# Kernel tuning notes

Measured on AMD Instinct MI355X. Metric: run time of the kernel, lower is better.

The kernel has to match this reference:

```python
import jax, jax.numpy as jnp
import numpy as np
from jax.scipy.special import logsumexp

SINKHORN_ITERS = 10


def _fix_coupling_sinkhorn(lc, lp1, lp2, iterations=SINKHORN_ITERS):
    # lc: [Z,S], lp1: [Z], lp2: [S]
    for _ in range(iterations):
        lc = lc + lp1[:, None] - logsumexp(lc, axis=1, keepdims=True)
        lc = lc + lp2[None, :] - logsumexp(lc, axis=0, keepdims=True)
    return lc


def _fix_coupling_rejection(lc, lp1, lp2):
    fixed_p1 = lc + lp1[:, None] - logsumexp(lc, axis=1, keepdims=True)
    approx_lp2 = logsumexp(fixed_p1, axis=0)
    accept = lp2 - approx_lp2
    accept = accept - jnp.max(accept)
    acc_s2_given_s1 = jax.nn.log_softmax(fixed_p1, axis=-1) + accept[None, :]
    log_keep = logsumexp(acc_s2_given_s1, axis=-1)
    certainly_keep = jnp.exp(log_keep) >= 1.0
    resample = jnp.where(
        certainly_keep, -jnp.inf,
        jnp.log1p(-jnp.where(certainly_keep, 0.0, jnp.exp(log_keep))))
    compensation = resample[:, None] + lp2[None, :]
    return lp1[:, None] + jnp.logaddexp(acc_s2_given_s1, compensation)


def setup_inputs() -> dict:
    key = jax.random.key(0)
    ks = jax.random.split(key, 8)
    B, S, Z, H1, H2 = 64, 512, 1024, 512, 256
    return {
        "s_logits": jax.random.normal(ks[0], (B, S), jnp.float32),
        "W1": jax.random.normal(ks[1], (S, H1), jnp.float32) / np.sqrt(S),
        "b1": jnp.zeros((H1,), jnp.float32),
        "W2": jax.random.normal(ks[2], (H1, H2), jnp.float32) / np.sqrt(H1),
        "b2": jnp.zeros((H2,), jnp.float32),
        "Wout": jax.random.normal(ks[3], (H2, Z, S), jnp.float32) / np.sqrt(H2),
        "bout": jnp.zeros((Z, S), jnp.float32),
        "prior": jax.random.normal(ks[4], (Z,), jnp.float32) * 0.05,
    }


def reference(s_logits, W1, b1, W2, b2, Wout, bout, prior):
    z_logits = jax.nn.log_softmax(prior)  # [Z]

    def get_joint(sl):  # sl: [S]
        v = jax.nn.softmax(sl)
        v = jax.nn.sigmoid(v @ W1 + b1)
        v = jax.nn.sigmoid(v @ W2 + b2)
        log_joint = jnp.einsum('h,hzs->zs', v, Wout) + bout  # [Z,S]
        log_joint = _fix_coupling_sinkhorn(log_joint, z_logits, sl)
        return _fix_coupling_rejection(log_joint, z_logits, sl)

    return jax.vmap(get_joint)(s_logits)  # [B,Z,S]
```

## Files before the change

kernel.cpp:

```cpp
#include <hip/hip_runtime.h>
#include <math.h>

#define Bn 64
#define Sn 512
#define Zn 1024
#define H1n 512
#define H2n 256
#define ZSn (Zn*Sn)

#define OFF_LP1  0
#define OFF_VT   1024
#define OFF_V    17408
#define OFF_W    50176
#define OFF_R    82944
#define OFF_PM   148480
#define OFF_PS   672768
#define OFF_KB   1310720
#define NEED_BF16_BYTES ((size_t)OFF_KB*4 + (size_t)Bn*ZSn*2)

#define NINF (-__builtin_inff())

__device__ __forceinline__ float wred_max(float x){
#pragma unroll
  for (int o=32;o;o>>=1) x = fmaxf(x, __shfl_xor(x, o, 64));
  return x;
}
__device__ __forceinline__ float wred_sum(float x){
#pragma unroll
  for (int o=32;o;o>>=1) x += __shfl_xor(x, o, 64);
  return x;
}
__device__ __forceinline__ float lae(float a, float c){
  float m = fmaxf(a,c), n = fminf(a,c);
  return m + log1pf(__expf(n-m));
}
__device__ __forceinline__ float toF(float v){ return v; }
__device__ __forceinline__ float toF(unsigned short v){ return __uint_as_float(((unsigned int)v)<<16); }
__device__ __forceinline__ unsigned int pack2(float a, float b){
  unsigned int ua = __float_as_uint(a), ub = __float_as_uint(b);
  ua = (ua + 0x7fffu + ((ua>>16)&1u)) >> 16;
  ub = (ub + 0x7fffu + ((ub>>16)&1u)) & 0xffff0000u;
  return ua | ub;
}

__global__ __launch_bounds__(512) void prep_kernel(const float* __restrict__ prior,
                                                   float* __restrict__ ws){
  __shared__ float red[8];
  int t = threadIdx.x;
  float x0 = prior[t], x1 = prior[t+512];
  float m = wred_max(fmaxf(x0,x1));
  if ((t&63)==0) red[t>>6] = m;
  __syncthreads();
  float M = red[0];
#pragma unroll
  for (int i=1;i<8;i++) M = fmaxf(M, red[i]);
  float e = __expf(x0-M)+__expf(x1-M);
  e = wred_sum(e);
  __syncthreads();
  if ((t&63)==0) red[t>>6] = e;
  __syncthreads();
  float T = 0.f;
#pragma unroll
  for (int i=0;i<8;i++) T += red[i];
  float lse = M + logf(T);
  ws[OFF_LP1 + t]       = x0 - lse;
  ws[OFF_LP1 + t + 512] = x1 - lse;
}

__global__ __launch_bounds__(512) void mlp_kernel(const float* __restrict__ sl,
    const float* __restrict__ W1, const float* __restrict__ b1,
    const float* __restrict__ W2, const float* __restrict__ b2,
    float* __restrict__ ws){
  __shared__ float p[Sn];
  __shared__ float h1s[H1n];
  __shared__ float red[8];
  int b = blockIdx.x, t = threadIdx.x;
  float x = sl[b*Sn + t];
  float m = wred_max(x);
  if ((t&63)==0) red[t>>6] = m;
  __syncthreads();
  float M = red[0];
#pragma unroll
  for (int i=1;i<8;i++) M = fmaxf(M, red[i]);
  float e = __expf(x-M);
  float es = wred_sum(e);
  __syncthreads();
  if ((t&63)==0) red[t>>6] = es;
  __syncthreads();
  float T = 0.f;
#pragma unroll
  for (int i=0;i<8;i++) T += red[i];
  p[t] = e / T;
  __syncthreads();
  float acc = b1[t];
#pragma unroll 8
  for (int s=0;s<Sn;s++) acc = fmaf(p[s], W1[s*H1n + t], acc);
  h1s[t] = 1.f/(1.f+__expf(-acc));
  __syncthreads();
  if (t < H2n){
    float a2 = b2[t];
#pragma unroll 8
    for (int s=0;s<H1n;s++) a2 = fmaf(h1s[s], W2[s*H2n + t], a2);
    ws[OFF_VT + t*Bn + b] = 1.f/(1.f+__expf(-a2));
  }
}

template<int BF>
__global__ __launch_bounds__(256,1) void gemm_kernel(const float* __restrict__ Wout,
    const float* __restrict__ bout, const float* __restrict__ ws,
    float* __restrict__ Kf, unsigned int* __restrict__ Kb){
  int zh = blockIdx.x*256 + threadIdx.x;
  const float* __restrict__ VT = ws + OFF_VT;
  float2 acc[Bn];
#pragma unroll
  for (int b=0;b<Bn;b++){ acc[b].x = 0.f; acc[b].y = 0.f; }
  const float2* Wp = (const float2*)Wout;
#pragma unroll 2
  for (int h=0; h<H2n; h++){
    float2 wv = Wp[(size_t)h*(ZSn/2) + zh];
    const float* vh = VT + (h<<6);
#pragma unroll
    for (int b=0;b<Bn;b++){
      acc[b].x = fmaf(vh[b], wv.x, acc[b].x);
      acc[b].y = fmaf(vh[b], wv.y, acc[b].y);
    }
  }
  float2 bb = ((const float2*)bout)[zh];
#pragma unroll
  for (int b=0;b<Bn;b++){
    float ax = acc[b].x + bb.x, ay = acc[b].y + bb.y;
    if (BF){
      Kb[(size_t)b*(ZSn/2) + zh] = pack2(ax, ay);
    } else {
      float2 o; o.x = ax; o.y = ay;
      ((float2*)Kf)[(size_t)b*(ZSn/2) + zh] = o;
    }
  }
}

template<typename KT>
__global__ __launch_bounds__(512) void iter_fused(const KT* __restrict__ Kg,
    float* __restrict__ ws, const float* __restrict__ sl, int iter, int mode){
  __shared__ KT Ksh[64*512];
  __shared__ float vsh[512];
  __shared__ float ush[64];
  __shared__ float lsh[64];
  int t = threadIdx.x;
  int b = blockIdx.x >> 4, c = blockIdx.x & 15;
  const float4* s4 = (const float4*)(Kg + ((size_t)((b<<10) + (c<<6)) << 9));
  float4* d4 = (float4*)Ksh;
  constexpr int NV = (int)sizeof(KT)*4;
#pragma unroll
  for (int i=0;i<NV;i++) d4[i*512 + t] = s4[i*512 + t];
  if (t < 64) lsh[t] = ws[OFF_LP1 + (c<<6) + t];
  float v_s;
  if (iter == 0) v_s = 0.f;
  else {
    float M = NINF, S = 0.f;
#pragma unroll
    for (int cc=0; cc<16; cc++){
      float m = ws[OFF_PM + ((b*16+cc)<<9) + t];
      float p = ws[OFF_PS + ((b*16+cc)<<9) + t];
      float nm = fmaxf(M, m);
      S = S*__expf(M-nm) + p*__expf(m-nm);
      M = nm;
    }
    v_s = sl[(b<<9) + t] - (M + logf(S));
  }
  vsh[t] = v_s;
  if (mode) ws[OFF_V + (b<<9) + t] = v_s;
  __syncthreads();
  int l = t & 63, w = t >> 6;
#pragma unroll
  for (int rr=0; rr<8; rr++){
    int row = (w<<3) + rr;
    float x[8];
    float m = NINF;
#pragma unroll
    for (int j=0;j<8;j++){
      x[j] = toF(Ksh[(row<<9) + (j<<6) + l]) + vsh[(j<<6)+l];
      m = fmaxf(m, x[j]);
    }
    m = wred_max(m);
    float s = 0.f;
#pragma unroll
    for (int j=0;j<8;j++) s += __expf(x[j]-m);
    s = wred_sum(s);
    float L = m + logf(s);
    if (l == 0){
      ush[row] = lsh[row] - L;
      if (mode) ws[OFF_R + (b<<10) + (c<<6) + row] = L;
    }
  }
  __syncthreads();
  float M = NINF, S = 0.f;
#pragma unroll 8
  for (int i=0;i<64;i++){
    float x2 = toF(Ksh[(i<<9) + t]) + ush[i];
    float nm = fmaxf(M, x2);
    S = S*__expf(M-nm) + __expf(x2-nm);
    M = nm;
  }
  ws[OFF_PM + ((b*16+c)<<9) + t] = M;
  ws[OFF_PS + ((b*16+c)<<9) + t] = S;
}

__global__ __launch_bounds__(512) void wker(float* __restrict__ ws, const float* __restrict__ sl){
  __shared__ float red[8];
  int b = blockIdx.x, s = threadIdx.x;
  float M = NINF, S = 0.f;
#pragma unroll
  for (int cc=0; cc<16; cc++){
    float m = ws[OFF_PM + ((b*16+cc)<<9) + s];
    float p = ws[OFF_PS + ((b*16+cc)<<9) + s];
    float nm = fmaxf(M, m);
    S = S*__expf(M-nm) + p*__expf(m-nm);
    M = nm;
  }
  float L = M + logf(S);
  float v = ws[OFF_V + (b<<9) + s];
  float araw = sl[(b<<9)+s] - v - L;
  float mm = wred_max(araw);
  if ((s&63)==0) red[s>>6] = mm;
  __syncthreads();
  float amax = red[0];
#pragma unroll
  for (int i=1;i<8;i++) amax = fmaxf(amax, red[i]);
  ws[OFF_W + (b<<9) + s] = v + araw - amax;
}

template<typename KT>
__global__ __launch_bounds__(512) void final_fused(const KT* Kg,
    float* out, const float* __restrict__ ws, const float* __restrict__ sl){
  int t = threadIdx.x, l = t & 63, wv = t >> 6;
  int row = blockIdx.x*8 + wv;
  int b = row >> 10, z = row & (Zn-1);
  const KT* Kr = Kg + ((size_t)row << 9);
  const float* wr = ws + OFF_W + (b << 9);
  const float* pr = sl + (b << 9);
  float r  = ws[OFF_R + row];
  float l1 = ws[OFF_LP1 + z];
  float k[8], a[8];
  float m = NINF;
#pragma unroll
  for (int j=0;j<8;j++){
    k[j] = toF(Kr[(j<<6)+l]);
    a[j] = k[j] - r + wr[(j<<6)+l];
    m = fmaxf(m, a[j]);
  }
  m = wred_max(m);
  float s = 0.f;
#pragma unroll
  for (int j=0;j<8;j++) s += __expf(a[j]-m);
  s = wred_sum(s);
  float lk = m + logf(s);
  float rs = (lk >= 0.f) ? NINF : log1pf(-__expf(lk));
  float* Or = out + ((size_t)row << 9);
#pragma unroll
  for (int j=0;j<8;j++){
    Or[(j<<6)+l] = l1 + lae(a[j], rs + pr[(j<<6)+l]);
  }
}

extern "C" void kernel_launch(void* const* d_in, const int* in_sizes, int n_in,
                              void* d_out, int out_size, void* d_ws, size_t ws_size,
                              hipStream_t stream) {
  const float* sl    = (const float*)d_in[0];
  const float* W1    = (const float*)d_in[1];
  const float* b1    = (const float*)d_in[2];
  const float* W2    = (const float*)d_in[3];
  const float* b2    = (const float*)d_in[4];
  const float* Wout  = (const float*)d_in[5];
  const float* bout  = (const float*)d_in[6];
  const float* prior = (const float*)d_in[7];
  float* ws = (float*)d_ws;
  float* Kf = (float*)d_out;
  unsigned short* Kb = (unsigned short*)(ws + OFF_KB);
  const bool use_bf16 = (ws_size >= NEED_BF16_BYTES);

  prep_kernel<<<1, 512, 0, stream>>>(prior, ws);
  mlp_kernel<<<Bn, 512, 0, stream>>>(sl, W1, b1, W2, b2, ws);

  if (use_bf16){
    gemm_kernel<1><<<ZSn/512, 256, 0, stream>>>(Wout, bout, ws, nullptr, (unsigned int*)Kb);
    for (int it = 0; it < 10; ++it)
      iter_fused<unsigned short><<<Bn*16, 512, 0, stream>>>(Kb, ws, sl, it, 0);
    iter_fused<unsigned short><<<Bn*16, 512, 0, stream>>>(Kb, ws, sl, 10, 1);
    wker<<<Bn, 512, 0, stream>>>(ws, sl);
    final_fused<unsigned short><<<Bn*Zn/8, 512, 0, stream>>>(Kb, (float*)d_out, ws, sl);
  } else {
    gemm_kernel<0><<<ZSn/512, 256, 0, stream>>>(Wout, bout, ws, Kf, nullptr);
    for (int it = 0; it < 10; ++it)
      iter_fused<float><<<Bn*16, 512, 0, stream>>>(Kf, ws, sl, it, 0);
    iter_fused<float><<<Bn*16, 512, 0, stream>>>(Kf, ws, sl, 10, 1);
    wker<<<Bn, 512, 0, stream>>>(ws, sl);
    final_fused<float><<<Bn*Zn/8, 512, 0, stream>>>(Kf, (float*)d_out, ws, sl);
  }
}
```

Measured before the change: 1.478 ms.

## Use bf16 MFMA for output GEMM and vectorize iteration and final kernels

Replaces the scalar FMA GEMM that produces the [B,Z,S] logit tensor with an MFMA 16x16x32 bf16 kernel. V is pre-rounded to bf16 in the MLP kernel, and Wout tiles are staged through LDS and converted to bf16 on the fly. The sinkhorn iteration kernel now reads LDS rows with 8-wide vector loads and splits the column online-logsumexp into two independent chains for more ILP. The final kernel uses float4 loads and stores. The GEMM inputs lose precision because both the activations and the weights are rounded to bf16 before multiplication.

Measured after the change: 1.326 ms. 10.3% less time.

```diff
diff --git a/kernel.cpp b/kernel.cpp
--- a/kernel.cpp
+++ b/kernel.cpp
@@ -15,10 +15,15 @@
 #define OFF_R    82944
 #define OFF_PM   148480
 #define OFF_PS   672768
+#define OFF_VB   1200128
 #define OFF_KB   1310720
 #define NEED_BF16_BYTES ((size_t)OFF_KB*4 + (size_t)Bn*ZSn*2)
 
 #define NINF (-__builtin_inff())
+
+typedef __attribute__((ext_vector_type(8))) short          s16x8;
+typedef __attribute__((ext_vector_type(8))) unsigned short u16x8;
+typedef __attribute__((ext_vector_type(4))) float          f32x4;
 
 __device__ __forceinline__ float wred_max(float x){
 #pragma unroll
@@ -36,6 +41,10 @@
 }
 __device__ __forceinline__ float toF(float v){ return v; }
 __device__ __forceinline__ float toF(unsigned short v){ return __uint_as_float(((unsigned int)v)<<16); }
+__device__ __forceinline__ unsigned short bf16rne(float f){
+  unsigned int u = __float_as_uint(f);
+  return (unsigned short)((u + 0x7fffu + ((u>>16)&1u)) >> 16);
+}
 __device__ __forceinline__ unsigned int pack2(float a, float b){
   unsigned int ua = __float_as_uint(a), ub = __float_as_uint(b);
   ua = (ua + 0x7fffu + ((ua>>16)&1u)) >> 16;
@@ -70,7 +79,7 @@
 __global__ __launch_bounds__(512) void mlp_kernel(const float* __restrict__ sl,
     const float* __restrict__ W1, const float* __restrict__ b1,
     const float* __restrict__ W2, const float* __restrict__ b2,
-    float* __restrict__ ws){
+    float* __restrict__ ws, int wbf){
   __shared__ float p[Sn];
   __shared__ float h1s[H1n];
   __shared__ float red[8];
@@ -101,7 +110,9 @@
     float a2 = b2[t];
 #pragma unroll 8
     for (int s=0;s<H1n;s++) a2 = fmaf(h1s[s], W2[s*H2n + t], a2);
-    ws[OFF_VT + t*Bn + b] = 1.f/(1.f+__expf(-a2));
+    float vv = 1.f/(1.f+__expf(-a2));
+    ws[OFF_VT + t*Bn + b] = vv;
+    if (wbf) ((unsigned short*)(ws + OFF_VB))[b*H2n + t] = bf16rne(vv);
   }
 }
 
@@ -134,6 +145,72 @@
     } else {
       float2 o; o.x = ax; o.y = ay;
       ((float2*)Kf)[(size_t)b*(ZSn/2) + zh] = o;
+    }
+  }
+}
+
+__global__ __launch_bounds__(256,3) void gemm_mfma(const float* __restrict__ Wout,
+    const float* __restrict__ bout, const float* __restrict__ ws,
+    unsigned short* __restrict__ Kb){
+  __shared__ unsigned short Vsh[64*264];
+  __shared__ float Bsh[32*65];
+  int t = threadIdx.x;
+  int zs0 = blockIdx.x * 64;
+
+  {
+    const unsigned short* vsrc = (const unsigned short*)(ws + OFF_VB);
+    int vrow = t >> 2, vq = t & 3;
+#pragma unroll
+    for (int i=0;i<8;i++)
+      *(u16x8*)&Vsh[vrow*264 + vq*64 + i*8] = *(const u16x8*)&vsrc[vrow*256 + vq*64 + i*8];
+  }
+
+  int w  = t >> 6;
+  int l  = t & 63;
+  int q  = l & 15;
+  int kg = l >> 4;
+  int sh = t >> 3, sf = t & 7;
+
+  float bo = bout[zs0 + (w<<4) + q];
+
+  f32x4 acc[4] = {{0.f,0.f,0.f,0.f},{0.f,0.f,0.f,0.f},{0.f,0.f,0.f,0.f},{0.f,0.f,0.f,0.f}};
+
+  const float4* src = (const float4*)(Wout + (size_t)sh * ZSn + zs0);
+  float4 ra = src[sf], rb = src[sf+8];
+
+  for (int ks=0; ks<8; ks++){
+    __syncthreads();
+    {
+      float* drow = &Bsh[sh*65 + (sf<<2)];
+      drow[0]=ra.x; drow[1]=ra.y; drow[2]=ra.z; drow[3]=ra.w;
+      drow[32]=rb.x; drow[33]=rb.y; drow[34]=rb.z; drow[35]=rb.w;
+    }
+    if (ks < 7){
+      const float4* s2 = (const float4*)(Wout + (size_t)((ks+1)*32 + sh) * ZSn + zs0);
+      ra = s2[sf]; rb = s2[sf+8];
+    }
+    __syncthreads();
+    float bf[8];
+#pragma unroll
+    for (int j=0;j<8;j++) bf[j] = Bsh[(kg*8+j)*65 + (w<<4) + q];
+    unsigned int pk[4];
+#pragma unroll
+    for (int j=0;j<4;j++)
+      asm("v_cvt_pk_bf16_f32 %0, %1, %2" : "=v"(pk[j]) : "v"(bf[2*j]), "v"(bf[2*j+1]));
+    union { unsigned int u[4]; s16x8 v; } bu;
+    bu.u[0]=pk[0]; bu.u[1]=pk[1]; bu.u[2]=pk[2]; bu.u[3]=pk[3];
+#pragma unroll
+    for (int mt=0; mt<4; mt++){
+      s16x8 af = *(const s16x8*)&Vsh[(mt*16 + q)*264 + ks*32 + kg*8];
+      acc[mt] = __builtin_amdgcn_mfma_f32_16x16x32_bf16(af, bu.v, acc[mt], 0, 0, 0);
+    }
+  }
+#pragma unroll
+  for (int mt=0; mt<4; mt++){
+#pragma unroll
+    for (int r=0; r<4; r++){
+      int b = mt*16 + kg*4 + r;
+      Kb[(size_t)b*ZSn + zs0 + (w<<4) + q] = bf16rne(acc[mt][r] + bo);
     }
   }
 }
@@ -171,16 +248,26 @@
   if (mode) ws[OFF_V + (b<<9) + t] = v_s;
   __syncthreads();
   int l = t & 63, w = t >> 6;
+  float vr[8];
+#pragma unroll
+  for (int j=0;j<8;j++) vr[j] = vsh[(l<<3)+j];
 #pragma unroll
   for (int rr=0; rr<8; rr++){
     int row = (w<<3) + rr;
     float x[8];
+    if constexpr (sizeof(KT)==2){
+      u16x8 kv = *(const u16x8*)&Ksh[(row<<9) + (l<<3)];
+#pragma unroll
+      for (int j=0;j<8;j++) x[j] = toF((unsigned short)kv[j]) + vr[j];
+    } else {
+      const float4* kp = (const float4*)&Ksh[(row<<9) + (l<<3)];
+      float4 k0 = kp[0], k1 = kp[1];
+      x[0]=k0.x+vr[0]; x[1]=k0.y+vr[1]; x[2]=k0.z+vr[2]; x[3]=k0.w+vr[3];
+      x[4]=k1.x+vr[4]; x[5]=k1.y+vr[5]; x[6]=k1.z+vr[6]; x[7]=k1.w+vr[7];
+    }
     float m = NINF;
 #pragma unroll
-    for (int j=0;j<8;j++){
-      x[j] = toF(Ksh[(row<<9) + (j<<6) + l]) + vsh[(j<<6)+l];
-      m = fmaxf(m, x[j]);
-    }
+    for (int j=0;j<8;j++) m = fmaxf(m, x[j]);
     m = wred_max(m);
     float s = 0.f;
 #pragma unroll
@@ -193,14 +280,20 @@
     }
   }
   __syncthreads();
-  float M = NINF, S = 0.f;
+  float M0 = NINF, S0 = 0.f, M1 = NINF, S1 = 0.f;
 #pragma unroll 8
-  for (int i=0;i<64;i++){
-    float x2 = toF(Ksh[(i<<9) + t]) + ush[i];
-    float nm = fmaxf(M, x2);
-    S = S*__expf(M-nm) + __expf(x2-nm);
-    M = nm;
-  }
+  for (int i=0;i<32;i++){
+    float xa = toF(Ksh[(i<<9) + t]) + ush[i];
+    float na = fmaxf(M0, xa);
+    S0 = S0*__expf(M0-na) + __expf(xa-na);
+    M0 = na;
+    float xb = toF(Ksh[((i+32)<<9) + t]) + ush[i+32];
+    float nb = fmaxf(M1, xb);
+    S1 = S1*__expf(M1-nb) + __expf(xb-nb);
+    M1 = nb;
+  }
+  float M = fmaxf(M0, M1);
+  float S = S0*__expf(M0-M) + S1*__expf(M1-M);
   ws[OFF_PM + ((b*16+c)<<9) + t] = M;
   ws[OFF_PS + ((b*16+c)<<9) + t] = S;
 }
@@ -230,8 +323,8 @@
 }
 
 template<typename KT>
-__global__ __launch_bounds__(512) void final_fused(const KT* Kg,
-    float* out, const float* __restrict__ ws, const float* __restrict__ sl){
+__global__ __launch_bounds__(512) void final_fused(const KT* __restrict__ Kg,
+    float* __restrict__ out, const float* __restrict__ ws, const float* __restrict__ sl){
   int t = threadIdx.x, l = t & 63, wv = t >> 6;
   int row = blockIdx.x*8 + wv;
   int b = row >> 10, z = row & (Zn-1);
@@ -240,12 +333,31 @@
   const float* pr = sl + (b << 9);
   float r  = ws[OFF_R + row];
   float l1 = ws[OFF_LP1 + z];
-  float k[8], a[8];
-  float m = NINF;
+  float ww[8], pp[8], kk[8];
+  {
+    const float4* wp = (const float4*)(wr + (l<<3));
+    float4 w0 = wp[0], w1 = wp[1];
+    ww[0]=w0.x; ww[1]=w0.y; ww[2]=w0.z; ww[3]=w0.w;
+    ww[4]=w1.x; ww[5]=w1.y; ww[6]=w1.z; ww[7]=w1.w;
+    const float4* pt = (const float4*)(pr + (l<<3));
+    float4 p0 = pt[0], p1 = pt[1];
+    pp[0]=p0.x; pp[1]=p0.y; pp[2]=p0.z; pp[3]=p0.w;
+    pp[4]=p1.x; pp[5]=p1.y; pp[6]=p1.z; pp[7]=p1.w;
+  }
+  if constexpr (sizeof(KT)==2){
+    u16x8 kv = *(const u16x8*)&Kr[l<<3];
+#pragma unroll
+    for (int j=0;j<8;j++) kk[j] = toF((unsigned short)kv[j]);
+  } else {
+    const float4* kp = (const float4*)&Kr[l<<3];
+    float4 k0 = kp[0], k1 = kp[1];
+    kk[0]=k0.x; kk[1]=k0.y; kk[2]=k0.z; kk[3]=k0.w;
+    kk[4]=k1.x; kk[5]=k1.y; kk[6]=k1.z; kk[7]=k1.w;
+  }
+  float a[8], m = NINF;
 #pragma unroll
   for (int j=0;j<8;j++){
-    k[j] = toF(Kr[(j<<6)+l]);
-    a[j] = k[j] - r + wr[(j<<6)+l];
+    a[j] = kk[j] - r + ww[j];
     m = fmaxf(m, a[j]);
   }
   m = wred_max(m);
@@ -255,11 +367,14 @@
   s = wred_sum(s);
   float lk = m + logf(s);
   float rs = (lk >= 0.f) ? NINF : log1pf(-__expf(lk));
-  float* Or = out + ((size_t)row << 9);
-#pragma unroll
-  for (int j=0;j<8;j++){
-    Or[(j<<6)+l] = l1 + lae(a[j], rs + pr[(j<<6)+l]);
-  }
+  float o[8];
+#pragma unroll
+  for (int j=0;j<8;j++) o[j] = l1 + lae(a[j], rs + pp[j]);
+  float4 o0, o1;
+  o0.x=o[0]; o0.y=o[1]; o0.z=o[2]; o0.w=o[3];
+  o1.x=o[4]; o1.y=o[5]; o1.z=o[6]; o1.w=o[7];
+  float4* op = (float4*)(out + ((size_t)row << 9) + (l<<3));
+  op[0] = o0; op[1] = o1;
 }
 
 extern "C" void kernel_launch(void* const* d_in, const int* in_sizes, int n_in,
@@ -279,10 +394,10 @@
   const bool use_bf16 = (ws_size >= NEED_BF16_BYTES);
 
   prep_kernel<<<1, 512, 0, stream>>>(prior, ws);
-  mlp_kernel<<<Bn, 512, 0, stream>>>(sl, W1, b1, W2, b2, ws);
+  mlp_kernel<<<Bn, 512, 0, stream>>>(sl, W1, b1, W2, b2, ws, use_bf16 ? 1 : 0);
 
   if (use_bf16){
-    gemm_kernel<1><<<ZSn/512, 256, 0, stream>>>(Wout, bout, ws, nullptr, (unsigned int*)Kb);
+    gemm_mfma<<<ZSn/64, 256, 0, stream>>>(Wout, bout, ws, Kb);
     for (int it = 0; it < 10; ++it)
       iter_fused<unsigned short><<<Bn*16, 512, 0, stream>>>(Kb, ws, sl, it, 0);
     iter_fused<unsigned short><<<Bn*16, 512, 0, stream>>>(Kb, ws, sl, 10, 1);
```
